# Kernel optimization log

Hardware: AMD Instinct MI355X
Metric: run time of the kernel (lower is better)

Reference implementation:

```python
import jax, jax.numpy as jnp
import numpy as np

N_NODES = 50000
N_EDGES = 800000
D_IN = 128
D_OUT = 128


def setup_inputs() -> dict:
    key = jax.random.key(0)
    k1, k2, k3, k4 = jax.random.split(key, 4)
    node_features = jax.random.normal(k1, (N_NODES, D_IN), dtype=jnp.float32)
    edge_index = jax.random.randint(k2, (2, N_EDGES), 0, N_NODES, dtype=jnp.int64)
    # nn.Linear params: weight [out, in], bias [out]
    W = jax.random.normal(k3, (D_OUT, D_IN), dtype=jnp.float32) / np.sqrt(D_IN)
    b = jax.random.normal(k4, (D_OUT,), dtype=jnp.float32) * 0.01
    return {"node_features": node_features, "edge_index": edge_index, "W": W, "b": b}


def reference(node_features, edge_index, W, b):
    source_nodes = edge_index[0]
    dest_nodes = edge_index[1]
    # gather neighbor features [E, D_in], scatter-add into [N, D_in]
    neighbor_features = node_features[source_nodes]
    aggregated = jax.ops.segment_sum(neighbor_features, dest_nodes,
                                     num_segments=node_features.shape[0])
    # nn.Linear: x @ W.T + b
    return aggregated @ W.T + b
```

## Files before the change

### kernel.cpp

```cpp
#include <hip/hip_runtime.h>


constexpr int NN = 50000;
constexpr int NE = 800000;
constexpr int D  = 128;

constexpr int BS   = 128;
constexpr int NB   = (NN + BS - 1) / BS;
constexpr int EPB  = 4096;
constexpr int NSB  = (NE + EPB - 1) / EPB;
constexpr int CAP  = 4096;

constexpr int AROWU = 136;

typedef __attribute__((ext_vector_type(8))) short bf16x8;
typedef __attribute__((ext_vector_type(4))) float f32x4;
typedef __attribute__((ext_vector_type(2))) float f32x2;

__device__ inline unsigned short f2bf(float f) {
    unsigned u = __float_as_uint(f);
    return (unsigned short)((u + 0x7fffu + ((u >> 16) & 1u)) >> 16);
}
__device__ inline float bflo(unsigned v) { return __uint_as_float(v << 16); }
__device__ inline float bfhi(unsigned v) { return __uint_as_float(v & 0xffff0000u); }

__device__ inline int wscan(int v) {
    #pragma unroll
    for (int o = 1; o < 64; o <<= 1) {
        int u = __shfl_up(v, o);
        if ((int)(threadIdx.x & 63) >= o) v += u;
    }
    return v;
}

__device__ inline void acc8(f32x2& a0, f32x2& a1, f32x2& a2, f32x2& a3, uint4 v) {
    a0 += (f32x2){bflo(v.x), bfhi(v.x)};
    a1 += (f32x2){bflo(v.y), bfhi(v.y)};
    a2 += (f32x2){bflo(v.z), bfhi(v.z)};
    a3 += (f32x2){bflo(v.w), bfhi(v.w)};
}

constexpr int NF4 = NN * D / 4;
constexpr int W4  = D * D / 4;
constexpr int NBLK_P = (NF4 + W4 + 511) / 512;
constexpr int GRID_A = NSB + NBLK_P;

__global__ __launch_bounds__(512) void k_prep_bucket(
    const float* __restrict__ nf, const float* __restrict__ W,
    const int* __restrict__ ei,
    ushort* __restrict__ nfh, ushort* __restrict__ Wh,
    ushort* __restrict__ offs, unsigned* __restrict__ buf)
{
    __shared__ int hist[NB], cur[NB];
    __shared__ int wsum[8];
    __shared__ unsigned spk[EPB];
    const int t = threadIdx.x, lane = t & 63, w = t >> 6;

    if (blockIdx.x < NSB) {
        const int blk = blockIdx.x;
        const int e0  = blk * EPB;
        int cnt = NE - e0; if (cnt > EPB) cnt = EPB;

        for (int i = t; i < NB; i += 512) hist[i] = 0;
        __syncthreads();

        unsigned pk[8];
        #pragma unroll
        for (int j = 0; j < 8; ++j) {
            int idx = j * 512 + t;
            if (idx < cnt) {
                int e = e0 + idx;
                unsigned s = (unsigned)ei[e];
                unsigned d = (unsigned)ei[NE + e];
                pk[j] = (d << 16) | s;
                atomicAdd(&hist[pk[j] >> 23], 1);
            }
        }
        __syncthreads();
        int h = (t < NB) ? hist[t] : 0;
        int v = wscan(h);
        if (lane == 63) wsum[w] = v;
        __syncthreads();
        int addv = 0;
        #pragma unroll
        for (int i = 0; i < 8; ++i) addv += (i < w) ? wsum[i] : 0;
        v += addv;
        if (t < NB) {
            int ex = v - h;
            cur[t] = ex;
            offs[t * NSB + blk] = (ushort)ex;
        }
        if (t == 0) offs[NB * NSB + blk] = (ushort)cnt;
        __syncthreads();
        #pragma unroll
        for (int j = 0; j < 8; ++j) {
            int idx = j * 512 + t;
            if (idx < cnt) {
                int l = atomicAdd(&cur[pk[j] >> 23], 1);
                spk[l] = pk[j];
            }
        }
        __syncthreads();
        for (int i = t; i < cnt; i += 512)
            buf[(size_t)blk * EPB + i] = spk[i];
    } else {
        int i = (blockIdx.x - NSB) * 512 + t;
        if (i < NF4) {
            float4 v = ((const float4*)nf)[i];
            ((ushort4*)nfh)[i] = make_ushort4(f2bf(v.x), f2bf(v.y), f2bf(v.z), f2bf(v.w));
        } else if (i < NF4 + W4) {
            int k = i - NF4;
            float4 v = ((const float4*)W)[k];
            ((ushort4*)Wh)[k] = make_ushort4(f2bf(v.x), f2bf(v.y), f2bf(v.z), f2bf(v.w));
        }
    }
}

__global__ __launch_bounds__(1024, 8) void k_sort_agg(
    const unsigned* __restrict__ nfh, const unsigned* __restrict__ buf,
    const ushort* __restrict__ offs, const ushort* __restrict__ Wh,
    const float* __restrict__ bias, float* __restrict__ out)
{
    __shared__ ushort srt[CAP];
    __shared__ int scnt[256];
    __shared__ int sbase[NSB], rbase[NSB];
    __shared__ int hist[BS], off[BS], cur[BS];
    __shared__ int wred[16];
    __shared__ __align__(16) unsigned tile[BS * AROWU / 2];
    const int b = blockIdx.x, t = threadIdx.x;
    const int lane = t & 63, w = t >> 6;

    int my = 0;
    if (t < NSB) {
        int o0 = (int)offs[b * NSB + t];
        int o1 = (int)offs[(b + 1) * NSB + t];
        rbase[t] = o0;
        my = o1 - o0;
    }
    if (t < BS) hist[t] = 0;
    int vs = 0;
    if (w < 4) {
        vs = wscan(my);
        if (lane == 63) wred[w] = vs;
    }
    __syncthreads();
    if (w < 4) {
        int addv = 0;
        #pragma unroll
        for (int i = 0; i < 3; ++i) addv += (i < w) ? wred[i] : 0;
        vs += addv;
        scnt[t] = vs;
        if (t < NSB) sbase[t] = vs - my;
    }
    __syncthreads();
    int total = scnt[NSB - 1];
    if (total > CAP) total = CAP;

    unsigned mypk[4];
    int mycnt = 0;
    #pragma unroll
    for (int j = 0; j < 4; ++j) {
        int p = t + j * 1024;
        if (p < total) {
            int lo = 0, hi = NSB - 1;
            while (lo < hi) {
                int mid = (lo + hi) >> 1;
                if (scnt[mid] > p) hi = mid; else lo = mid + 1;
            }
            unsigned pk = buf[(size_t)lo * EPB + rbase[lo] + (p - sbase[lo])];
            mypk[j] = pk;
            atomicAdd(&hist[(pk >> 16) & (BS - 1)], 1);
            mycnt = j + 1;
        }
    }
    __syncthreads();

    int hv = (t < BS) ? hist[t] : 0;
    int nv = 0;
    if (w < 2) {
        nv = wscan(hv);
        if (lane == 63) wred[8 + w] = nv;
    }
    __syncthreads();
    if (t < BS) {
        int ex = nv + ((w == 1) ? wred[8] : 0) - hv;
        off[t] = ex; cur[t] = ex;
    }
    __syncthreads();
    #pragma unroll
    for (int j = 0; j < 4; ++j) {
        if (j < mycnt) {
            unsigned pk = mypk[j];
            int n = (pk >> 16) & (BS - 1);
            int p = atomicAdd(&cur[n], 1);
            srt[p] = (ushort)(pk & 0xffffu);
        }
    }
    __syncthreads();

    const int qq = lane >> 4;
    const int sl = lane & 15;
    const uint4* nfv = (const uint4*)nfh;

    #pragma unroll 1
    for (int i = 0; i < 2; ++i) {
        const int n = w * 8 + i * 4 + qq;
        const int beg = off[n], cnt = hist[n];
        f32x2 a0 = {0.f, 0.f}, a1 = {0.f, 0.f}, a2 = {0.f, 0.f}, a3 = {0.f, 0.f};
        int p = 0;
        for (; p + 2 <= cnt; p += 2) {
            const int s0 = srt[beg + p];
            const int s1 = srt[beg + p + 1];
            const uint4 v0 = nfv[(size_t)s0 * 16 + sl];
            const uint4 v1 = nfv[(size_t)s1 * 16 + sl];
            acc8(a0, a1, a2, a3, v0);
            acc8(a0, a1, a2, a3, v1);
        }
        if (p < cnt) {
            const int s0 = srt[beg + p];
            const uint4 v0 = nfv[(size_t)s0 * 16 + sl];
            acc8(a0, a1, a2, a3, v0);
        }
        uint4 o;
        o.x = (unsigned)f2bf(a0.x) | ((unsigned)f2bf(a0.y) << 16);
        o.y = (unsigned)f2bf(a1.x) | ((unsigned)f2bf(a1.y) << 16);
        o.z = (unsigned)f2bf(a2.x) | ((unsigned)f2bf(a2.y) << 16);
        o.w = (unsigned)f2bf(a3.x) | ((unsigned)f2bf(a3.y) << 16);
        *(uint4*)(tile + n * (AROWU / 2) + sl * 4) = o;
    }
    __syncthreads();

    const int m = lane & 15, q = lane >> 4;
    const ushort* lds = (const ushort*)tile;
    #pragma unroll
    for (int i = 0; i < 4; ++i) {
        const int task = w + 16 * i;
        const int t16  = task >> 3;
        const int c0   = (task & 7) * 16;
        const int grow0 = b * BS + t16 * 16;
        if (grow0 < NN) {
            bf16x8 a[4];
            const ushort* arow = lds + (t16 * 16 + m) * AROWU + q * 8;
            #pragma unroll
            for (int kk = 0; kk < 4; ++kk)
                a[kk] = *(const bf16x8*)(arow + kk * 32);
            float bv = bias[c0 + m];
            f32x4 acc = { bv, bv, bv, bv };
            const ushort* wrow = Wh + (size_t)(c0 + m) * D + q * 8;
            #pragma unroll
            for (int kk = 0; kk < 4; ++kk) {
                bf16x8 bb = *(const bf16x8*)(wrow + kk * 32);
                acc = __builtin_amdgcn_mfma_f32_16x16x32_bf16(a[kk], bb, acc, 0, 0, 0);
            }
            float* op = out + (size_t)(grow0 + q * 4) * D + c0 + m;
            op[0]     = acc[0];
            op[D]     = acc[1];
            op[2 * D] = acc[2];
            op[3 * D] = acc[3];
        }
    }
}

extern "C" void kernel_launch(void* const* d_in, const int* in_sizes, int n_in,
                              void* d_out, int out_size, void* d_ws, size_t ws_size,
                              hipStream_t stream) {
    const float* nf = (const float*)d_in[0];
    const int*   ei = (const int*)d_in[1];
    const float* W  = (const float*)d_in[2];
    const float* b  = (const float*)d_in[3];
    float* out = (float*)d_out;

    ushort*   nfh  = (ushort*)d_ws;
    ushort*   Wh   = nfh + (size_t)NN * D;
    unsigned* buf  = (unsigned*)(Wh + D * D);
    ushort*   offs = (ushort*)(buf + (size_t)NSB * EPB);

    k_prep_bucket<<<GRID_A, 512, 0, stream>>>(nf, W, ei, nfh, Wh, offs, buf);
    k_sort_agg   <<<NB, 1024, 0, stream>>>((const unsigned*)nfh, buf, offs, Wh, b, out);
}
```

Before: 128.3 us.

## Stream neighbor rows into LDS with async global_load_lds double buffering

Halves the node bucket size to 64 and runs the sort/aggregate kernel with 512 threads. The gather of neighbor feature rows now uses async global-to-LDS loads into per-wave double-buffered staging, with explicit vmcnt waits. Each wave walks its contiguous edge range across its 8 nodes instead of one node per 16-lane group. This aims to overlap gather latency with accumulation, at the cost of serialized per-wave accumulation (each lane holds 2 columns), more blocks, and a smaller per-block capacity (CAP 2048).

```diff
diff --git a/kernel.cpp b/kernel.cpp
--- a/kernel.cpp
+++ b/kernel.cpp
@@ -5,11 +5,11 @@
 constexpr int NE = 800000;
 constexpr int D  = 128;
 
-constexpr int BS   = 128;
+constexpr int BS   = 64;
 constexpr int NB   = (NN + BS - 1) / BS;
 constexpr int EPB  = 4096;
 constexpr int NSB  = (NE + EPB - 1) / EPB;
-constexpr int CAP  = 4096;
+constexpr int CAP  = 2048;
 
 constexpr int AROWU = 136;
 
@@ -33,12 +33,15 @@
     return v;
 }
 
-__device__ inline void acc8(f32x2& a0, f32x2& a1, f32x2& a2, f32x2& a3, uint4 v) {
-    a0 += (f32x2){bflo(v.x), bfhi(v.x)};
-    a1 += (f32x2){bflo(v.y), bfhi(v.y)};
-    a2 += (f32x2){bflo(v.z), bfhi(v.z)};
-    a3 += (f32x2){bflo(v.w), bfhi(v.w)};
-}
+__device__ __forceinline__ void gl_lds16(const unsigned* g, unsigned* l) {
+    __builtin_amdgcn_global_load_lds(
+        (const __attribute__((address_space(1))) unsigned*)g,
+        (__attribute__((address_space(3))) unsigned*)l, 16, 0, 0);
+}
+#define WAITVM2() { asm volatile("s_waitcnt vmcnt(2)" ::: "memory"); \
+                    __builtin_amdgcn_sched_barrier(0); }
+#define WAITVM0() { asm volatile("s_waitcnt vmcnt(0)" ::: "memory"); \
+                    __builtin_amdgcn_sched_barrier(0); }
 
 constexpr int NF4 = NN * D / 4;
 constexpr int W4  = D * D / 4;
@@ -73,30 +76,30 @@
                 unsigned s = (unsigned)ei[e];
                 unsigned d = (unsigned)ei[NE + e];
                 pk[j] = (d << 16) | s;
-                atomicAdd(&hist[pk[j] >> 23], 1);
-            }
-        }
-        __syncthreads();
-        int h = (t < NB) ? hist[t] : 0;
-        int v = wscan(h);
+                atomicAdd(&hist[pk[j] >> 22], 1);
+            }
+        }
+        __syncthreads();
+        const int i0 = 2 * t, i1 = 2 * t + 1;
+        int h0 = (i0 < NB) ? hist[i0] : 0;
+        int h1 = (i1 < NB) ? hist[i1] : 0;
+        int v = wscan(h0 + h1);
         if (lane == 63) wsum[w] = v;
         __syncthreads();
         int addv = 0;
         #pragma unroll
         for (int i = 0; i < 8; ++i) addv += (i < w) ? wsum[i] : 0;
         v += addv;
-        if (t < NB) {
-            int ex = v - h;
-            cur[t] = ex;
-            offs[t * NSB + blk] = (ushort)ex;
-        }
+        int ex1 = v - h1, ex0 = ex1 - h0;
+        if (i0 < NB) { cur[i0] = ex0; offs[i0 * NSB + blk] = (ushort)ex0; }
+        if (i1 < NB) { cur[i1] = ex1; offs[i1 * NSB + blk] = (ushort)ex1; }
         if (t == 0) offs[NB * NSB + blk] = (ushort)cnt;
         __syncthreads();
         #pragma unroll
         for (int j = 0; j < 8; ++j) {
             int idx = j * 512 + t;
             if (idx < cnt) {
-                int l = atomicAdd(&cur[pk[j] >> 23], 1);
+                int l = atomicAdd(&cur[pk[j] >> 22], 1);
                 spk[l] = pk[j];
             }
         }
@@ -116,7 +119,7 @@
     }
 }
 
-__global__ __launch_bounds__(1024, 8) void k_sort_agg(
+__global__ __launch_bounds__(512, 4) void k_sort_agg(
     const unsigned* __restrict__ nfh, const unsigned* __restrict__ buf,
     const ushort* __restrict__ offs, const ushort* __restrict__ Wh,
     const float* __restrict__ bias, float* __restrict__ out)
@@ -127,6 +130,7 @@
     __shared__ int hist[BS], off[BS], cur[BS];
     __shared__ int wred[16];
     __shared__ __align__(16) unsigned tile[BS * AROWU / 2];
+    __shared__ __align__(16) unsigned stag[8][1024];
     const int b = blockIdx.x, t = threadIdx.x;
     const int lane = t & 63, w = t >> 6;
 
@@ -160,7 +164,7 @@
     int mycnt = 0;
     #pragma unroll
     for (int j = 0; j < 4; ++j) {
-        int p = t + j * 1024;
+        int p = t + j * 512;
         if (p < total) {
             int lo = 0, hi = NSB - 1;
             while (lo < hi) {
@@ -177,15 +181,9 @@
 
     int hv = (t < BS) ? hist[t] : 0;
     int nv = 0;
-    if (w < 2) {
-        nv = wscan(hv);
-        if (lane == 63) wred[8 + w] = nv;
-    }
-    __syncthreads();
-    if (t < BS) {
-        int ex = nv + ((w == 1) ? wred[8] : 0) - hv;
-        off[t] = ex; cur[t] = ex;
-    }
+    if (w == 0) nv = wscan(hv);
+    __syncthreads();
+    if (t < BS) { int ex = nv - hv; off[t] = ex; cur[t] = ex; }
     __syncthreads();
     #pragma unroll
     for (int j = 0; j < 4; ++j) {
@@ -198,43 +196,66 @@
     }
     __syncthreads();
 
-    const int qq = lane >> 4;
-    const int sl = lane & 15;
-    const uint4* nfv = (const uint4*)nfh;
-
-    #pragma unroll 1
-    for (int i = 0; i < 2; ++i) {
-        const int n = w * 8 + i * 4 + qq;
-        const int beg = off[n], cnt = hist[n];
-        f32x2 a0 = {0.f, 0.f}, a1 = {0.f, 0.f}, a2 = {0.f, 0.f}, a3 = {0.f, 0.f};
-        int p = 0;
-        for (; p + 2 <= cnt; p += 2) {
-            const int s0 = srt[beg + p];
-            const int s1 = srt[beg + p + 1];
-            const uint4 v0 = nfv[(size_t)s0 * 16 + sl];
-            const uint4 v1 = nfv[(size_t)s1 * 16 + sl];
-            acc8(a0, a1, a2, a3, v0);
-            acc8(a0, a1, a2, a3, v1);
-        }
-        if (p < cnt) {
-            const int s0 = srt[beg + p];
-            const uint4 v0 = nfv[(size_t)s0 * 16 + sl];
-            acc8(a0, a1, a2, a3, v0);
-        }
-        uint4 o;
-        o.x = (unsigned)f2bf(a0.x) | ((unsigned)f2bf(a0.y) << 16);
-        o.y = (unsigned)f2bf(a1.x) | ((unsigned)f2bf(a1.y) << 16);
-        o.z = (unsigned)f2bf(a2.x) | ((unsigned)f2bf(a2.y) << 16);
-        o.w = (unsigned)f2bf(a3.x) | ((unsigned)f2bf(a3.y) << 16);
-        *(uint4*)(tile + n * (AROWU / 2) + sl * 4) = o;
-    }
+    const int qw = lane >> 4;
+    const int slw = lane & 15;
+    const unsigned* nfu = nfh;
+    unsigned* stagw = stag[w];
+
+    const int wbeg = off[w * 8];
+    const int wend = (w < 7) ? off[w * 8 + 8] : total;
+    const int nq = wend - wbeg;
+    const int nc = (nq + 7) >> 3;
+
+    auto ISSUE = [&](int c) {
+        const int half = (c & 1) * 512;
+        #pragma unroll
+        for (int j = 0; j < 2; ++j) {
+            int e = wbeg + c * 8 + j * 4 + qw;
+            if (e >= wend) e = wbeg;
+            const unsigned* g = nfu + (size_t)srt[e] * 64 + slw * 4;
+            gl_lds16(g, stagw + half + j * 256);
+        }
+    };
+    auto ENDR = [&](int cn_) -> int {
+        int n1 = w * 8 + cn_ + 1;
+        return ((n1 < BS) ? off[n1] : total) - wbeg;
+    };
+
+    f32x2 acc = {0.f, 0.f};
+    int cn = 0;
+    int cend = ENDR(0);
+
+    if (nc > 0) {
+        ISSUE(0);
+        if (nc > 1) ISSUE(1);
+        for (int c = 0; c < nc; ++c) {
+            if (c + 1 < nc) { WAITVM2(); } else { WAITVM0(); }
+            int kmax = nq - 8 * c; if (kmax > 8) kmax = 8;
+            for (int k = 0; k < kmax; ++k) {
+                int p = 8 * c + k;
+                while (cn < 7 && p >= cend) {
+                    tile[(w * 8 + cn) * (AROWU / 2) + lane] =
+                        (unsigned)f2bf(acc.x) | ((unsigned)f2bf(acc.y) << 16);
+                    acc.x = 0.f; acc.y = 0.f;
+                    ++cn; cend = ENDR(cn);
+                }
+                unsigned u = stagw[((p & 15) << 6) + lane];
+                acc.x += bflo(u); acc.y += bfhi(u);
+            }
+            if (c + 2 < nc) ISSUE(c + 2);
+        }
+    }
+    tile[(w * 8 + cn) * (AROWU / 2) + lane] =
+        (unsigned)f2bf(acc.x) | ((unsigned)f2bf(acc.y) << 16);
+    for (int z = cn + 1; z < 8; ++z)
+        tile[(w * 8 + z) * (AROWU / 2) + lane] = 0u;
     __syncthreads();
 
     const int m = lane & 15, q = lane >> 4;
     const ushort* lds = (const ushort*)tile;
     #pragma unroll
     for (int i = 0; i < 4; ++i) {
-        const int task = w + 16 * i;
+        const int task = w + 8 * i;
         const int t16  = task >> 3;
         const int c0   = (task & 7) * 16;
         const int grow0 = b * BS + t16 * 16;
@@ -245,18 +266,18 @@
             for (int kk = 0; kk < 4; ++kk)
                 a[kk] = *(const bf16x8*)(arow + kk * 32);
             float bv = bias[c0 + m];
-            f32x4 acc = { bv, bv, bv, bv };
+            f32x4 acc4 = { bv, bv, bv, bv };
             const ushort* wrow = Wh + (size_t)(c0 + m) * D + q * 8;
             #pragma unroll
             for (int kk = 0; kk < 4; ++kk) {
                 bf16x8 bb = *(const bf16x8*)(wrow + kk * 32);
-                acc = __builtin_amdgcn_mfma_f32_16x16x32_bf16(a[kk], bb, acc, 0, 0, 0);
+                acc4 = __builtin_amdgcn_mfma_f32_16x16x32_bf16(a[kk], bb, acc4, 0, 0, 0);
             }
             float* op = out + (size_t)(grow0 + q * 4) * D + c0 + m;
-            op[0]     = acc[0];
-            op[D]     = acc[1];
-            op[2 * D] = acc[2];
-            op[3 * D] = acc[3];
+            op[0]     = acc4[0];
+            op[D]     = acc4[1];
+            op[2 * D] = acc4[2];
+            op[3 * D] = acc4[3];
         }
     }
 }
@@ -276,5 +297,5 @@
     ushort*   offs = (ushort*)(buf + (size_t)NSB * EPB);
 
     k_prep_bucket<<<GRID_A, 512, 0, stream>>>(nf, W, ei, nfh, Wh, offs, buf);
-    k_sort_agg   <<<NB, 1024, 0, stream>>>((const unsigned*)nfh, buf, offs, Wh, b, out);
-}
+    k_sort_agg   <<<NB, 512, 0, stream>>>((const unsigned*)nfh, buf, offs, Wh, b, out);
+}
```

Measured after the change: 150.3 us. 17.2% more time.
